# Kernel tuning notes

Measured on AMD Instinct MI355X. Metric: run time of the kernel, lower is better.

## Reference

```python
import jax, jax.numpy as jnp
import numpy as np

B, S, D = 2, 2048, 1024
H = 16
HD = D // H


def setup_inputs() -> dict:
    key = jax.random.key(0)
    ks = jax.random.split(key, 6)
    X = jax.random.normal(ks[0], (B, S, D), dtype=jnp.float32)
    # Linear weights stored [in, out] so y = x @ W (torch stores transposed).
    sc = 1.0 / np.sqrt(D)
    Wq = jax.random.normal(ks[1], (D, D), dtype=jnp.float32) * sc
    Wk = jax.random.normal(ks[2], (D, D), dtype=jnp.float32) * sc
    Wv = jax.random.normal(ks[3], (D, D), dtype=jnp.float32) * sc
    Wo = jax.random.normal(ks[4], (D, D), dtype=jnp.float32) * sc
    bo = jax.random.normal(ks[5], (D,), dtype=jnp.float32) * 0.01
    return {"X": X, "Wq": Wq, "Wk": Wk, "Wv": Wv, "Wo": Wo, "bo": bo}


def reference(X, Wq, Wk, Wv, Wo, bo):
    b, n, _ = X.shape
    # QKV projections (no bias, qkv_bias=False), reshape to [b, h, n, hd]
    q = (X @ Wq).reshape(b, n, H, HD).transpose(0, 2, 1, 3)
    k = (X @ Wk).reshape(b, n, H, HD).transpose(0, 2, 1, 3)
    v = (X @ Wv).reshape(b, n, H, HD).transpose(0, 2, 1, 3)
    # Unscaled scores (module's scale flag defaults to False)
    scores = jnp.einsum("bhqd,bhkd->bhqk", q, k)
    causal = jnp.triu(jnp.ones((n, n), dtype=bool), k=1)  # True above diagonal
    scores = jnp.where(causal, -jnp.inf, scores)
    attn = jax.nn.softmax(scores, axis=-1)
    # dropout p=0.0 -> identity
    ctx = jnp.einsum("bhqk,bhkd->bqhd", attn, v).reshape(b, n, H * HD)
    return ctx @ Wo + bo
```

## Files before the change

kernel.cpp:

```cpp
#include <hip/hip_runtime.h>
#include <stdint.h>


typedef __attribute__((ext_vector_type(8))) short short8;
typedef __attribute__((ext_vector_type(4))) float floatx4;

#define S_LEN 2048
#define D_DIM 1024
#define NH 16
#define HD 64
#define L2E 1.44269504088896340736f

__device__ __forceinline__ short f2bf(float f) {
    uint32_t u = __builtin_bit_cast(uint32_t, f);
    uint32_t r = u + 0x7fffu + ((u >> 16) & 1u);
    return (short)(r >> 16);
}
__device__ __forceinline__ uint32_t pack2(float a, float b) {
#if __has_builtin(__builtin_amdgcn_cvt_pk_bf16_f32)
    auto v = __builtin_amdgcn_cvt_pk_bf16_f32(a, b);
    uint32_t r; __builtin_memcpy(&r, &v, sizeof(r)); return r;
#else
    return (uint32_t)(uint16_t)f2bf(a) | ((uint32_t)(uint16_t)f2bf(b) << 16);
#endif
}
__device__ __forceinline__ void gll16(const void* g, void* l) {
    __builtin_amdgcn_global_load_lds(
        (const __attribute__((address_space(1))) void*)g,
        (__attribute__((address_space(3))) void*)l, 16, 0, 0);
}

__global__ __launch_bounds__(256) void castx_kernel(const float* __restrict__ X,
                                                    short* __restrict__ Xb) {
    int i = blockIdx.x * 256 + threadIdx.x;
    const float4 v = *(const float4*)(X + (size_t)i * 4);
    uint2 o;
    o.x = pack2(v.x, v.y);
    o.y = pack2(v.z, v.w);
    *(uint2*)(Xb + (size_t)i * 4) = o;
}

__global__ __launch_bounds__(256) void tcast4_kernel(const float* __restrict__ Wq,
                                                     const float* __restrict__ Wk,
                                                     const float* __restrict__ Wv,
                                                     const float* __restrict__ Wo,
                                                     short* __restrict__ WqkvT,
                                                     short* __restrict__ WoT) {
    const int z = blockIdx.z;
    const float* W = (z == 0) ? Wq : (z == 1) ? Wk : (z == 2) ? Wv : Wo;
    short* WT = (z < 3) ? (WqkvT + (size_t)z * 1024 * 1024) : WoT;
    __shared__ float tile[32][33];
    const int bx = blockIdx.x * 32;
    const int by = blockIdx.y * 32;
    const int tx = threadIdx.x, ty = threadIdx.y;
    for (int i = 0; i < 32; i += 8)
        tile[ty + i][tx] = W[(size_t)(bx + ty + i) * D_DIM + by + tx];
    __syncthreads();
    for (int i = 0; i < 32; i += 8)
        WT[(size_t)(by + ty + i) * D_DIM + bx + tx] = f2bf(tile[tx][ty + i]);
}

__device__ __forceinline__ void gemm_main8(const short* __restrict__ A,
                                           const short* __restrict__ BT,
                                           short* As, short* Bs,
                                           int m0, int n0, floatx4 (&acc)[4][2],
                                           int tid) {
    const int lane = tid & 63, ln = lane & 15, quad = lane >> 4;
    const int wave = tid >> 6;
    const int mw = (wave & 1) * 64, nw = (wave >> 1) * 32;
    for (int k0 = 0; k0 < D_DIM; k0 += 64) {
        __syncthreads();
        for (int t = 0; t < 2; t++) {
            const int c = t * 512 + tid;
            const int row = c >> 3, pos = c & 7, src = pos ^ (row & 7);
            gll16(A  + (size_t)(m0 + row) * D_DIM + k0 + src * 8, As + c * 8);
            gll16(BT + (size_t)(n0 + row) * D_DIM + k0 + src * 8, Bs + c * 8);
        }
        __syncthreads();
        for (int ks = 0; ks < 2; ks++) {
            short8 a[4], b[2];
            for (int i = 0; i < 4; i++) {
                const int row = mw + i * 16 + ln;
                a[i] = *(const short8*)(As + row * 64 + (((ks * 4 + quad) ^ (ln & 7)) * 8));
            }
            for (int j = 0; j < 2; j++) {
                const int row = nw + j * 16 + ln;
                b[j] = *(const short8*)(Bs + row * 64 + (((ks * 4 + quad) ^ (ln & 7)) * 8));
            }
            for (int i = 0; i < 4; i++)
                for (int j = 0; j < 2; j++)
                    acc[i][j] = __builtin_amdgcn_mfma_f32_16x16x32_bf16(a[i], b[j], acc[i][j], 0, 0, 0);
        }
    }
}

__global__ __launch_bounds__(512) void gemm_qkv_kernel(const short* __restrict__ Xb,
                                                       const short* __restrict__ WT,
                                                       short* __restrict__ Qb,
                                                       short* __restrict__ Kb,
                                                       short* __restrict__ Vtb) {
    __shared__ __align__(16) short As[128 * 64];
    __shared__ __align__(16) short Bs[128 * 64];
    const int m0 = blockIdx.x * 128, n0 = blockIdx.y * 128;
    floatx4 acc[4][2] = {};
    gemm_main8(Xb, WT, As, Bs, m0, n0, acc, threadIdx.x);

    const int tid = threadIdx.x, wave = tid >> 6, lane = tid & 63;
    const int ln = lane & 15, quad = lane >> 4;
    const int mw = (wave & 1) * 64, nw = (wave >> 1) * 32;
    const int nsel = n0 >> 10;
    const float qs = (nsel == 0) ? L2E : 1.f;
    short* outB = (nsel == 0) ? Qb : (nsel == 1 ? Kb : Vtb);
    for (int i = 0; i < 4; i++)
        for (int j = 0; j < 2; j++)
            for (int r = 0; r < 4; r++) {
                const int row = m0 + mw + i * 16 + quad * 4 + r;
                const int col = (n0 & 1023) + nw + j * 16 + ln;
                const int bb = row >> 11, s = row & (S_LEN - 1);
                const int h = col >> 6, hd = col & (HD - 1);
                const short v = f2bf(acc[i][j][r] * qs);
                if (nsel < 2)
                    outB[(((size_t)(bb * NH + h)) * S_LEN + s) * HD + hd] = v;
                else
                    outB[(((size_t)(bb * NH + h)) * HD + hd) * S_LEN + s] = v;
            }
}

__global__ __launch_bounds__(512) void gemm_out_kernel(const short* __restrict__ Cb,
                                                       const short* __restrict__ WoT,
                                                       float* __restrict__ out,
                                                       const float* __restrict__ bias) {
    __shared__ __align__(16) short As[128 * 64];
    __shared__ __align__(16) short Bs[64 * 64];
    const int m0 = blockIdx.x * 128, n0 = blockIdx.y * 64;
    const int tid = threadIdx.x, lane = tid & 63;
    const int ln = lane & 15, quad = lane >> 4;
    const int wave = tid >> 6;
    const int mw = (wave & 3) * 32, nw = (wave >> 2) * 32;

    floatx4 acc[2][2] = {};

    for (int k0 = 0; k0 < D_DIM; k0 += 64) {
        __syncthreads();
        for (int t = 0; t < 2; t++) {
            const int c = t * 512 + tid;
            const int row = c >> 3, pos = c & 7, src = pos ^ (row & 7);
            gll16(Cb + (size_t)(m0 + row) * D_DIM + k0 + src * 8, As + c * 8);
        }
        {
            const int c = tid;
            const int row = c >> 3, pos = c & 7, src = pos ^ (row & 7);
            gll16(WoT + (size_t)(n0 + row) * D_DIM + k0 + src * 8, Bs + c * 8);
        }
        __syncthreads();
        for (int ks = 0; ks < 2; ks++) {
            short8 a[2], b[2];
            for (int i = 0; i < 2; i++) {
                const int row = mw + i * 16 + ln;
                a[i] = *(const short8*)(As + row * 64 + (((ks * 4 + quad) ^ (ln & 7)) * 8));
            }
            for (int j = 0; j < 2; j++) {
                const int row = nw + j * 16 + ln;
                b[j] = *(const short8*)(Bs + row * 64 + (((ks * 4 + quad) ^ (ln & 7)) * 8));
            }
            for (int i = 0; i < 2; i++)
                for (int j = 0; j < 2; j++)
                    acc[i][j] = __builtin_amdgcn_mfma_f32_16x16x32_bf16(a[i], b[j], acc[i][j], 0, 0, 0);
        }
    }

    for (int i = 0; i < 2; i++)
        for (int j = 0; j < 2; j++)
            for (int r = 0; r < 4; r++) {
                const int row = m0 + mw + i * 16 + quad * 4 + r;
                const int col = n0 + nw + j * 16 + ln;
                out[(size_t)row * D_DIM + col] = acc[i][j][r] + bias[col];
            }
}

__global__ __launch_bounds__(512, 4) void attn_kernel(const short* __restrict__ Q,
                                                      const short* __restrict__ Kg,
                                                      const short* __restrict__ Vt,
                                                      short* __restrict__ ctx,
                                                      float* __restrict__ Opart,
                                                      float* __restrict__ Lpart) {
    __shared__ __align__(16) short Ks[128 * 64];
    __shared__ __align__(16) short Vs[64 * 128];
    __shared__ __align__(16) short Ps[8][1280];

    const int tid = threadIdx.x, wave = tid >> 6, lane = tid & 63;
    const int ln = lane & 15, quad = lane >> 4;

    const int id = blockIdx.x;
    const int bh = (id & 7) + 8 * ((id >> 3) & 3);
    const int t = id >> 5;

    static const unsigned char TASK[24] = {
        0xF0, 0x02, 0xF1, 0x12, 0xE1, 0x22, 0x72, 0x80,
        0xE0, 0x32, 0xD0, 0xA0, 0xD1, 0x90, 0xC1, 0x91,
        0xC0, 0x81, 0xB0, 0x42, 0xB1, 0xA1, 0x62, 0x52};
    const int code = TASK[t];
    const int qt = code >> 4, mode = code & 3;
    const int n = qt + 1, h0 = n >> 1;
    const int k_begin = (mode == 1) ? h0 : 0;
    const int k_end   = (mode == 0) ? h0 : n;
    const int pidx    = (mode == 2) ? -1 : ((qt - 8) * 32 + bh) * 2 + mode;
    const int kmask = qt;
    const int q0 = qt * 128;
    const int bb = bh >> 4, h = bh & 15;
    short* Pw = Ps[wave];

    const short* qrow = Q + ((size_t)bh * S_LEN + q0 + wave * 16 + ln) * HD;
    const short8 qb0 = *(const short8*)(qrow + quad * 8);
    const short8 qb1 = *(const short8*)(qrow + 32 + quad * 8);
    const int q_abs = q0 + wave * 16 + ln;

    float l_part = 0.f;
    floatx4 o_acc[4] = {};

    for (int kt = k_begin; kt < k_end; kt++) {
        const int k0 = kt * 128;
        __syncthreads();
        for (int tt = 0; tt < 2; tt++) {
            const int c = tt * 512 + tid;
            {
                const int row = c >> 3, pos = c & 7, src = pos ^ (row & 7);
                gll16(Kg + ((size_t)bh * S_LEN + k0 + row) * HD + src * 8, Ks + c * 8);
            }
            {
                const int row = c >> 4, pos = c & 15, src = pos ^ (row & 15);
                gll16(Vt + ((size_t)bh * HD + row) * S_LEN + k0 + src * 8, Vs + c * 8);
            }
        }
        __syncthreads();

        floatx4 sc[8];
        __builtin_amdgcn_s_setprio(1);
        for (int nt = 0; nt < 8; nt++) {
            const int row = nt * 16 + ln;
            const short8 ak0 = *(const short8*)(Ks + row * 64 + ((quad ^ (ln & 7)) * 8));
            const short8 ak1 = *(const short8*)(Ks + row * 64 + (((4 + quad) ^ (ln & 7)) * 8));
            floatx4 z = {};
            z = __builtin_amdgcn_mfma_f32_16x16x32_bf16(ak0, qb0, z, 0, 0, 0);
            z = __builtin_amdgcn_mfma_f32_16x16x32_bf16(ak1, qb1, z, 0, 0, 0);
            sc[nt] = z;
        }
        __builtin_amdgcn_s_setprio(0);

        if (kt == kmask) {
            for (int nt = 0; nt < 8; nt++)
                for (int r = 0; r < 4; r++)
                    if (k0 + nt * 16 + quad * 4 + r > q_abs) sc[nt][r] = -1e30f;
        }

        float ls = 0.f;
        for (int nt = 0; nt < 8; nt++)
            for (int r = 0; r < 4; r++) {
                const float e = exp2f(sc[nt][r]);
                sc[nt][r] = e; ls += e;
            }
        l_part += ls;

        for (int p = 0; p < 4; p++) {
            short* Pq = Pw + (p & 1) * 640;
            uint2 u0, u1;
            u0.x = pack2(sc[2 * p][0], sc[2 * p][1]);
            u0.y = pack2(sc[2 * p][2], sc[2 * p][3]);
            u1.x = pack2(sc[2 * p + 1][0], sc[2 * p + 1][1]);
            u1.y = pack2(sc[2 * p + 1][2], sc[2 * p + 1][3]);
            *(uint2*)&Pq[ln * 40 + quad * 4]      = u0;
            *(uint2*)&Pq[ln * 40 + 16 + quad * 4] = u1;
            const short8 bp = *(const short8*)&Pq[ln * 40 + quad * 8];
            __builtin_amdgcn_s_setprio(1);
            for (int dt = 0; dt < 4; dt++) {
                const int row = dt * 16 + ln;
                const short8 av = *(const short8*)(Vs + row * 128 + (((p * 4 + quad) ^ (ln & 15)) * 8));
                o_acc[dt] = __builtin_amdgcn_mfma_f32_16x16x32_bf16(av, bp, o_acc[dt], 0, 0, 0);
            }
            __builtin_amdgcn_s_setprio(0);
        }
    }

    float l_tot = l_part;
    l_tot += __shfl_xor(l_tot, 16, 64);
    l_tot += __shfl_xor(l_tot, 32, 64);

    if (pidx >= 0) {
        float* Ob = Opart + (size_t)pidx * 8192 + (wave * 16 + ln) * 64;
        for (int dt = 0; dt < 4; dt++)
            *(float4*)(Ob + dt * 16 + quad * 4) = *(float4*)&o_acc[dt];
        if (quad == 0) Lpart[(size_t)pidx * 128 + wave * 16 + ln] = l_tot;
    } else {
        const float rl = 1.f / l_tot;
        for (int dt = 0; dt < 4; dt++) {
            uint2 u;
            u.x = pack2(o_acc[dt][0] * rl, o_acc[dt][1] * rl);
            u.y = pack2(o_acc[dt][2] * rl, o_acc[dt][3] * rl);
            *(uint2*)&Pw[(dt >> 1) * 640 + ln * 40 + (dt & 1) * 16 + quad * 4] = u;
        }
        const int qr = lane >> 2, sg = lane & 3;
        for (int c = 0; c < 2; c++) {
            const short8 v = *(const short8*)&Pw[c * 640 + qr * 40 + sg * 8];
            const int s = q0 + wave * 16 + qr;
            *(short8*)(ctx + ((size_t)bb * S_LEN + s) * D_DIM + h * HD + sg * 8 + c * 32) = v;
        }
    }
}

__global__ __launch_bounds__(256) void combine_kernel(const float* __restrict__ Opart,
                                                      const float* __restrict__ Lpart,
                                                      short* __restrict__ ctx) {
    const int tile = blockIdx.x;
    const int qt = 8 + (tile >> 5), bh = tile & 31;
    const int bb = bh >> 4, h = bh & 15;
    const int p0 = ((qt - 8) * 32 + bh) * 2;
    const float* O0 = Opart + (size_t)p0 * 8192;
    const float* O1 = O0 + 8192;
    const float* l0 = Lpart + (size_t)p0 * 128;
    const float* l1 = l0 + 128;
    for (int e = threadIdx.x; e < 2048; e += 256) {
        const int q = e >> 4, seg = e & 15;
        const float rl = 1.f / (l0[q] + l1[q]);
        const float4 x0 = *(const float4*)(O0 + q * 64 + seg * 4);
        const float4 x1 = *(const float4*)(O1 + q * 64 + seg * 4);
        uint2 u;
        u.x = pack2((x0.x + x1.x) * rl, (x0.y + x1.y) * rl);
        u.y = pack2((x0.z + x1.z) * rl, (x0.w + x1.w) * rl);
        const int s = qt * 128 + q;
        *(uint2*)(ctx + ((size_t)bb * S_LEN + s) * D_DIM + h * HD + seg * 4) = u;
    }
}

extern "C" void kernel_launch(void* const* d_in, const int* in_sizes, int n_in,
                              void* d_out, int out_size, void* d_ws, size_t ws_size,
                              hipStream_t stream) {
    const float* X  = (const float*)d_in[0];
    const float* Wq = (const float*)d_in[1];
    const float* Wk = (const float*)d_in[2];
    const float* Wv = (const float*)d_in[3];
    const float* Wo = (const float*)d_in[4];
    const float* bo = (const float*)d_in[5];
    float* out = (float*)d_out;

    char* ws = (char*)d_ws;
    const size_t MB = 1024 * 1024;
    short* Xb     = (short*)(ws);
    short* WqkvT  = (short*)(ws + 8  * MB);
    short* Qb     = (short*)(ws + 16 * MB);
    short* Kb     = (short*)(ws + 24 * MB);
    short* Vtb    = (short*)(ws + 32 * MB);
    short* ctxb   = (short*)(ws + 40 * MB);
    short* WoT    = (short*)(ws + 48 * MB);
    float* Opart  = (float*)(ws);
    float* Lpart  = (float*)(ws + 50 * MB);

    castx_kernel<<<4096, 256, 0, stream>>>(X, Xb);
    dim3 tg(32, 32, 4), tb(32, 8);
    tcast4_kernel<<<tg, tb, 0, stream>>>(Wq, Wk, Wv, Wo, WqkvT, WoT);

    dim3 gq(32, 24);
    gemm_qkv_kernel<<<gq, 512, 0, stream>>>(Xb, WqkvT, Qb, Kb, Vtb);

    attn_kernel<<<768, 512, 0, stream>>>(Qb, Kb, Vtb, ctxb, Opart, Lpart);
    combine_kernel<<<256, 256, 0, stream>>>(Opart, Lpart, ctxb);

    dim3 go(32, 16);
    gemm_out_kernel<<<go, 512, 0, stream>>>(ctxb, WoT, out, bo);
}
```

Baseline: 188.5 us.

## Double-buffer 64-key K/V tiles in attention with async prefetch

The attention loop now walks 64-key tiles instead of 128-key tiles and keeps two LDS buffers for K and V. The next tile's global-to-LDS loads are issued before computing on the current one, with explicit vmcnt waits and raw barriers, so memory latency can overlap with the MFMA work. Shrinking the tile and the P scratch lets the launch bound go from 4 to 6 blocks per CU for higher occupancy. In exchange there are twice as many loop iterations and barriers, and the causal mask now applies to two tiles per diagonal block.

```diff
diff --git a/kernel.cpp b/kernel.cpp
--- a/kernel.cpp
+++ b/kernel.cpp
@@ -178,15 +178,15 @@
             }
 }
 
-__global__ __launch_bounds__(512, 4) void attn_kernel(const short* __restrict__ Q,
+__global__ __launch_bounds__(512, 6) void attn_kernel(const short* __restrict__ Q,
                                                       const short* __restrict__ Kg,
                                                       const short* __restrict__ Vt,
                                                       short* __restrict__ ctx,
                                                       float* __restrict__ Opart,
                                                       float* __restrict__ Lpart) {
-    __shared__ __align__(16) short Ks[128 * 64];
-    __shared__ __align__(16) short Vs[64 * 128];
-    __shared__ __align__(16) short Ps[8][1280];
+    __shared__ __align__(16) short Ks[2][64 * 64];
+    __shared__ __align__(16) short Vs[2][64 * 64];
+    __shared__ __align__(16) short Ps[8][640];
 
     const int tid = threadIdx.x, wave = tid >> 6, lane = tid & 63;
     const int ln = lane & 15, quad = lane >> 4;
@@ -202,10 +202,10 @@
     const int code = TASK[t];
     const int qt = code >> 4, mode = code & 3;
     const int n = qt + 1, h0 = n >> 1;
-    const int k_begin = (mode == 1) ? h0 : 0;
-    const int k_end   = (mode == 0) ? h0 : n;
-    const int pidx    = (mode == 2) ? -1 : ((qt - 8) * 32 + bh) * 2 + mode;
-    const int kmask = qt;
+    const int kb = 2 * ((mode == 1) ? h0 : 0);
+    const int ke = 2 * ((mode == 0) ? h0 : n);
+    const int pidx   = (mode == 2) ? -1 : ((qt - 8) * 32 + bh) * 2 + mode;
+    const int kmask0 = 2 * qt;
     const int q0 = qt * 128;
     const int bb = bh >> 4, h = bh & 15;
     short* Pw = Ps[wave];
@@ -215,71 +215,88 @@
     const short8 qb1 = *(const short8*)(qrow + 32 + quad * 8);
     const int q_abs = q0 + wave * 16 + ln;
 
+    const int srow = tid >> 3, spos = tid & 7, ssrc = spos ^ (srow & 7);
+    const size_t kbase = (size_t)bh * S_LEN * HD;
+    const size_t vbase = (size_t)bh * HD * S_LEN;
+
     float l_part = 0.f;
     floatx4 o_acc[4] = {};
 
-    for (int kt = k_begin; kt < k_end; kt++) {
-        const int k0 = kt * 128;
-        __syncthreads();
-        for (int tt = 0; tt < 2; tt++) {
-            const int c = tt * 512 + tid;
-            {
-                const int row = c >> 3, pos = c & 7, src = pos ^ (row & 7);
-                gll16(Kg + ((size_t)bh * S_LEN + k0 + row) * HD + src * 8, Ks + c * 8);
-            }
-            {
-                const int row = c >> 4, pos = c & 15, src = pos ^ (row & 15);
-                gll16(Vt + ((size_t)bh * HD + row) * S_LEN + k0 + src * 8, Vs + c * 8);
-            }
-        }
-        __syncthreads();
-
-        floatx4 sc[8];
+#define STAGE(buf, kt_)                                                          \
+    {                                                                            \
+        const int k0s = (kt_) * 64;                                              \
+        gll16(Kg + kbase + (size_t)(k0s + srow) * HD + ssrc * 8,                 \
+              &Ks[buf][tid * 8]);                                                \
+        gll16(Vt + vbase + (size_t)srow * S_LEN + k0s + ssrc * 8,                \
+              &Vs[buf][tid * 8]);                                                \
+    }
+
+    int cur = 0;
+    STAGE(0, kb);
+    for (int kt = kb; kt < ke; kt++) {
+        if (kt + 1 < ke) {
+            STAGE(cur ^ 1, kt + 1);
+            asm volatile("s_waitcnt vmcnt(2)" ::: "memory");
+        } else {
+            asm volatile("s_waitcnt vmcnt(0)" ::: "memory");
+        }
+        __builtin_amdgcn_s_barrier();
+        __builtin_amdgcn_sched_barrier(0);
+
+        const short* Kc = Ks[cur];
+        const short* Vc = Vs[cur];
+
+        floatx4 sc4[4];
         __builtin_amdgcn_s_setprio(1);
-        for (int nt = 0; nt < 8; nt++) {
+        for (int nt = 0; nt < 4; nt++) {
             const int row = nt * 16 + ln;
-            const short8 ak0 = *(const short8*)(Ks + row * 64 + ((quad ^ (ln & 7)) * 8));
-            const short8 ak1 = *(const short8*)(Ks + row * 64 + (((4 + quad) ^ (ln & 7)) * 8));
+            const short8 ak0 = *(const short8*)(Kc + row * 64 + ((quad ^ (ln & 7)) * 8));
+            const short8 ak1 = *(const short8*)(Kc + row * 64 + (((4 + quad) ^ (ln & 7)) * 8));
             floatx4 z = {};
             z = __builtin_amdgcn_mfma_f32_16x16x32_bf16(ak0, qb0, z, 0, 0, 0);
             z = __builtin_amdgcn_mfma_f32_16x16x32_bf16(ak1, qb1, z, 0, 0, 0);
-            sc[nt] = z;
+            sc4[nt] = z;
         }
         __builtin_amdgcn_s_setprio(0);
 
-        if (kt == kmask) {
-            for (int nt = 0; nt < 8; nt++)
+        if (kt >= kmask0) {
+            const int k0 = kt * 64;
+            for (int nt = 0; nt < 4; nt++)
                 for (int r = 0; r < 4; r++)
-                    if (k0 + nt * 16 + quad * 4 + r > q_abs) sc[nt][r] = -1e30f;
+                    if (k0 + nt * 16 + quad * 4 + r > q_abs) sc4[nt][r] = -1e30f;
         }
 
         float ls = 0.f;
-        for (int nt = 0; nt < 8; nt++)
+        for (int nt = 0; nt < 4; nt++)
             for (int r = 0; r < 4; r++) {
-                const float e = exp2f(sc[nt][r]);
-                sc[nt][r] = e; ls += e;
+                const float e = exp2f(sc4[nt][r]);
+                sc4[nt][r] = e; ls += e;
             }
         l_part += ls;
 
-        for (int p = 0; p < 4; p++) {
-            short* Pq = Pw + (p & 1) * 640;
+        for (int p = 0; p < 2; p++) {
             uint2 u0, u1;
-            u0.x = pack2(sc[2 * p][0], sc[2 * p][1]);
-            u0.y = pack2(sc[2 * p][2], sc[2 * p][3]);
-            u1.x = pack2(sc[2 * p + 1][0], sc[2 * p + 1][1]);
-            u1.y = pack2(sc[2 * p + 1][2], sc[2 * p + 1][3]);
-            *(uint2*)&Pq[ln * 40 + quad * 4]      = u0;
-            *(uint2*)&Pq[ln * 40 + 16 + quad * 4] = u1;
-            const short8 bp = *(const short8*)&Pq[ln * 40 + quad * 8];
+            u0.x = pack2(sc4[2 * p][0], sc4[2 * p][1]);
+            u0.y = pack2(sc4[2 * p][2], sc4[2 * p][3]);
+            u1.x = pack2(sc4[2 * p + 1][0], sc4[2 * p + 1][1]);
+            u1.y = pack2(sc4[2 * p + 1][2], sc4[2 * p + 1][3]);
+            *(uint2*)&Pw[ln * 40 + quad * 4]      = u0;
+            *(uint2*)&Pw[ln * 40 + 16 + quad * 4] = u1;
+            const short8 bp = *(const short8*)&Pw[ln * 40 + quad * 8];
             __builtin_amdgcn_s_setprio(1);
             for (int dt = 0; dt < 4; dt++) {
                 const int row = dt * 16 + ln;
-                const short8 av = *(const short8*)(Vs + row * 128 + (((p * 4 + quad) ^ (ln & 15)) * 8));
+                const short8 av = *(const short8*)(Vc + row * 64 + (((p * 4 + quad) ^ (ln & 7)) * 8));
                 o_acc[dt] = __builtin_amdgcn_mfma_f32_16x16x32_bf16(av, bp, o_acc[dt], 0, 0, 0);
             }
             __builtin_amdgcn_s_setprio(0);
         }
-    }
+
+        __builtin_amdgcn_sched_barrier(0);
+        __builtin_amdgcn_s_barrier();
+        cur ^= 1;
+    }
+#undef STAGE
 
     float l_tot = l_part;
     l_tot += __shfl_xor(l_tot, 16, 64);
@@ -292,15 +309,16 @@
         if (quad == 0) Lpart[(size_t)pidx * 128 + wave * 16 + ln] = l_tot;
     } else {
         const float rl = 1.f / l_tot;
-        for (int dt = 0; dt < 4; dt++) {
-            uint2 u;
-            u.x = pack2(o_acc[dt][0] * rl, o_acc[dt][1] * rl);
-            u.y = pack2(o_acc[dt][2] * rl, o_acc[dt][3] * rl);
-            *(uint2*)&Pw[(dt >> 1) * 640 + ln * 40 + (dt & 1) * 16 + quad * 4] = u;
-        }
         const int qr = lane >> 2, sg = lane & 3;
         for (int c = 0; c < 2; c++) {
-            const short8 v = *(const short8*)&Pw[c * 640 + qr * 40 + sg * 8];
+            for (int dd = 0; dd < 2; dd++) {
+                const int dt = c * 2 + dd;
+                uint2 u;
+                u.x = pack2(o_acc[dt][0] * rl, o_acc[dt][1] * rl);
+                u.y = pack2(o_acc[dt][2] * rl, o_acc[dt][3] * rl);
+                *(uint2*)&Pw[ln * 40 + dd * 16 + quad * 4] = u;
+            }
+            const short8 v = *(const short8*)&Pw[qr * 40 + sg * 8];
             const int s = q0 + wave * 16 + qr;
             *(short8*)(ctx + ((size_t)bb * S_LEN + s) * D_DIM + h * HD + sg * 8 + c * 32) = v;
         }
```

Measured after the change: 190.8 us. No clear change (+1.2%).
